# Kernel optimization log

Measured on AMD Instinct MI355X. Metric: run time of the kernel, lower is better.

## Reference

```python
import jax, jax.numpy as jnp
import numpy as np

N = 32768; D = 384; P = 3; CORR_D = 2 * 49 * P * P  # 882
G_KK = 4096; G_JK = 512
EPS = 1e-3  # LayerNorm eps in the torch module

FLOAT_NAMES = ("net","inp","corr","corr_w1","corr_b1","corr_w2","corr_b2","corr_ln_g","corr_ln_b","corr_w3","corr_b3","norm_g","norm_b","c1_w1","c1_b1","c1_w2","c1_b2","c2_w1","c2_b1","c2_w2","c2_b2","kk_fw","kk_fb","kk_gw","kk_gb","kk_hw","kk_hb","ij_fw","ij_fb","ij_gw","ij_gb","ij_hw","ij_hb","g_ln1_g","g_ln1_b","g1_gw","g1_gb","g1_r1w","g1_r1b","g1_r2w","g1_r2b","g_ln2_g","g_ln2_b","g2_gw","g2_gb","g2_r1w","g2_r1b","g2_r2w","g2_r2b","d_w","d_b","w_w","w_b")

def _ln(x, g, b):
    m = jnp.mean(x, -1, keepdims=True)
    v = jnp.mean((x - m) ** 2, -1, keepdims=True)
    return (x - m) * jax.lax.rsqrt(v + EPS) * g + b

def _mlp2(x, w1, b1, w2, b2):
    return jax.nn.relu(x @ w1 + b1) @ w2 + b2

def _gated_residual(x, gw, gb, r1w, r1b, r2w, r2b):
    gate = jax.nn.sigmoid(x @ gw + gb)
    res = jax.nn.relu(x @ r1w + r1b) @ r2w + r2b
    return x + gate * res

def _soft_agg(x, jx, fw, fb, gw, gb, hw, hb, num_groups):
    # x: [N, D]; jx: [N] group ids -> group-wise softmax weighted sum
    logits = x @ gw + gb
    feats = x @ fw + fb
    gmax = jax.ops.segment_max(logits, jx, num_segments=num_groups)
    e = jnp.exp(logits - gmax[jx])
    den = jax.ops.segment_sum(e, jx, num_segments=num_groups)
    w = e / (den[jx] + 1e-12)
    y = jax.ops.segment_sum(feats * w, jx, num_segments=num_groups)
    return (y @ hw + hb)[jx]

def _forward(p, nix, njx, ukk, ujk):
    # corr encoder MLP
    h = jax.nn.relu(p["corr"] @ p["corr_w1"] + p["corr_b1"]) @ p["corr_w2"] + p["corr_b2"]
    h = jax.nn.relu(_ln(h, p["corr_ln_g"], p["corr_ln_b"])) @ p["corr_w3"] + p["corr_b3"]
    net = p["net"] + p["inp"] + h
    net = _ln(net, p["norm_g"], p["norm_b"])
    mask_ix = (nix >= 0).astype(net.dtype).reshape(1, -1, 1)
    mask_jx = (njx >= 0).astype(net.dtype).reshape(1, -1, 1)
    net = net + _mlp2(mask_ix * net[:, nix], p["c1_w1"], p["c1_b1"], p["c1_w2"], p["c1_b2"])
    net = net + _mlp2(mask_jx * net[:, njx], p["c2_w1"], p["c2_b1"], p["c2_w2"], p["c2_b2"])
    net = net + _soft_agg(net[0], ukk, p["kk_fw"], p["kk_fb"], p["kk_gw"], p["kk_gb"], p["kk_hw"], p["kk_hb"], G_KK)[None]
    net = net + _soft_agg(net[0], ujk, p["ij_fw"], p["ij_fb"], p["ij_gw"], p["ij_gb"], p["ij_hw"], p["ij_hb"], G_JK)[None]
    net = _ln(net, p["g_ln1_g"], p["g_ln1_b"])
    net = _gated_residual(net, p["g1_gw"], p["g1_gb"], p["g1_r1w"], p["g1_r1b"], p["g1_r2w"], p["g1_r2b"])
    net = _ln(net, p["g_ln2_g"], p["g_ln2_b"])
    net = _gated_residual(net, p["g2_gw"], p["g2_gb"], p["g2_r1w"], p["g2_r1b"], p["g2_r2w"], p["g2_r2b"])
    r = jax.nn.relu(net)
    d = r @ p["d_w"] + p["d_b"]               # GradClip is identity in forward
    w = jax.nn.sigmoid(r @ p["w_w"] + p["w_b"])
    return net, d, w

def setup_inputs() -> dict:
    key = jax.random.key(0)
    it = iter(jax.random.split(key, 64))
    def pr(*shape):
        return jax.random.normal(next(it), shape, dtype=jnp.float32) * 0.02
    z = lambda *s: jnp.zeros(s, jnp.float32)
    o = lambda *s: jnp.ones(s, jnp.float32)
    inp = {
        "net": jax.random.normal(next(it), (1, N, D), dtype=jnp.float32),
        "inp": jax.random.normal(next(it), (1, N, D), dtype=jnp.float32),
        "corr": jax.random.normal(next(it), (1, N, CORR_D), dtype=jnp.float32),
        "nix": jax.random.randint(next(it), (N,), 0, N),
        "njx": jax.random.randint(next(it), (N,), 0, N),
        "ukk": jax.random.randint(next(it), (N,), 0, G_KK),
        "ujk": jax.random.randint(next(it), (N,), 0, G_JK),
        "corr_w1": pr(CORR_D, D), "corr_b1": z(D), "corr_w2": pr(D, D), "corr_b2": z(D),
        "corr_ln_g": o(D), "corr_ln_b": z(D), "corr_w3": pr(D, D), "corr_b3": z(D),
        "norm_g": o(D), "norm_b": z(D),
        "c1_w1": pr(D, D), "c1_b1": z(D), "c1_w2": pr(D, D), "c1_b2": z(D),
        "c2_w1": pr(D, D), "c2_b1": z(D), "c2_w2": pr(D, D), "c2_b2": z(D),
        "kk_fw": pr(D, D), "kk_fb": z(D), "kk_gw": pr(D, D), "kk_gb": z(D), "kk_hw": pr(D, D), "kk_hb": z(D),
        "ij_fw": pr(D, D), "ij_fb": z(D), "ij_gw": pr(D, D), "ij_gb": z(D), "ij_hw": pr(D, D), "ij_hb": z(D),
        "g_ln1_g": o(D), "g_ln1_b": z(D),
        "g1_gw": pr(D, D), "g1_gb": z(D), "g1_r1w": pr(D, D), "g1_r1b": z(D), "g1_r2w": pr(D, D), "g1_r2b": z(D),
        "g_ln2_g": o(D), "g_ln2_b": z(D),
        "g2_gw": pr(D, D), "g2_gb": z(D), "g2_r1w": pr(D, D), "g2_r1b": z(D), "g2_r2w": pr(D, D), "g2_r2b": z(D),
        "d_w": pr(D, 2), "d_b": z(2), "w_w": pr(D, 2), "w_b": z(2),
    }
    return inp

def reference(net, inp, corr, corr_w1, corr_b1, corr_w2, corr_b2, corr_ln_g, corr_ln_b, corr_w3, corr_b3, norm_g, norm_b, c1_w1, c1_b1, c1_w2, c1_b2, c2_w1, c2_b1, c2_w2, c2_b2, kk_fw, kk_fb, kk_gw, kk_gb, kk_hw, kk_hb, ij_fw, ij_fb, ij_gw, ij_gb, ij_hw, ij_hb, g_ln1_g, g_ln1_b, g1_gw, g1_gb, g1_r1w, g1_r1b, g1_r2w, g1_r2b, g_ln2_g, g_ln2_b, g2_gw, g2_gb, g2_r1w, g2_r1b, g2_r2w, g2_r2b, d_w, d_b, w_w, w_b, nix, njx, ukk, ujk):
    loc = locals()
    fl = {k: loc[k] for k in FLOAT_NAMES}
    return _forward(fl, nix, njx, ukk, ujk)
```

## Files before the change

kernel.cpp:

```cpp
#include <hip/hip_runtime.h>
#include <hip/hip_bf16.h>
#include <math.h>

#define NR 32768
#define DD 384
#define CDM 882
#define CDMP 896

typedef float f4 __attribute__((ext_vector_type(4)));
typedef float f32x4 __attribute__((ext_vector_type(4)));
typedef __bf16 bf16x8 __attribute__((ext_vector_type(8)));
typedef __bf16 bf16x4 __attribute__((ext_vector_type(4)));

__device__ inline f4 ld4(const float* p) { f4 v; __builtin_memcpy(&v, p, 16); return v; }
__device__ inline void st4(float* p, f4 v) { __builtin_memcpy(p, &v, 16); }
__device__ inline bf16x8 ld8h(const __bf16* p) { bf16x8 v; __builtin_memcpy(&v, p, 16); return v; }
__device__ inline void st8h(__bf16* p, bf16x8 v) { __builtin_memcpy(p, &v, 16); }

__device__ inline void gl_lds16(const void* g, void* l) {
  __builtin_amdgcn_global_load_lds(
      (const __attribute__((address_space(1))) void*)g,
      (__attribute__((address_space(3))) void*)l, 16, 0, 0);
}

__device__ inline float gred16(float v) {
#pragma unroll
  for (int o = 1; o < 16; o <<= 1) v += __shfl_xor(v, o, 64);
  return v;
}

__device__ inline int xcd_swz(int orig, int nwg) {
  int q = nwg >> 3, r = nwg & 7, xcd = orig & 7, lid = orig >> 3;
  return (xcd < r ? xcd * (q + 1) : r * (q + 1) + (xcd - r) * q) + lid;
}

__global__ __launch_bounds__(256) void corr2bf16_k(const float* __restrict__ src,
                                                   __bf16* __restrict__ dst) {
  int i = blockIdx.x * 256 + threadIdx.x;
  int row = i / 112, c8 = (i - row * 112) * 8;
  const float* sp = src + (size_t)row * CDM + c8;
  bf16x8 h;
  if (c8 + 8 <= CDM) {
#pragma unroll
    for (int e = 0; e < 8; ++e) h[e] = (__bf16)sp[e];
  } else {
#pragma unroll
    for (int e = 0; e < 8; ++e) h[e] = (c8 + e < CDM) ? (__bf16)sp[e] : (__bf16)0.f;
  }
  st8h(dst + (size_t)row * CDMP + c8, h);
}

struct WPtrs { const float* w[18]; };

__global__ __launch_bounds__(256) void trans_all_k(WPtrs P, __bf16* __restrict__ dst) {
  int wi = blockIdx.y;
  const float* W = P.w[wi];
  __bf16* WT = dst + (size_t)wi * DD * DD;
  int i = blockIdx.x * 256 + threadIdx.x;
  if (i >= DD * DD) return;
  int n = i / DD, k = i - n * DD;
  WT[i] = (__bf16)W[(size_t)k * DD + n];
}

__global__ __launch_bounds__(256) void trans_corr_k(const float* __restrict__ W,
                                                    __bf16* __restrict__ WT) {
  int i = blockIdx.x * 256 + threadIdx.x;
  if (i >= DD * CDMP) return;
  int n = i / CDMP, k = i - n * CDMP;
  WT[i] = (k < CDM) ? (__bf16)W[(size_t)k * DD + n] : (__bf16)0.f;
}

struct GP {
  const void* A; const __bf16* WT; const float* bias; __bf16* OUT;
  const __bf16* XRES; const __bf16* GIN;
  const float* p0; const float* p1; const float* p2; const float* p3;
  float* fout; const float* net32; const float* inp32;
  const int* idx; const __bf16* zpage; int M; int K;
};

template <int EPI>
__device__ __forceinline__ void epilogue(const GP& gp, f32x4 (&acc)[4][6],
                                         __bf16* sm, int m0, int w, int lane) {
  const int fr = lane & 15, fq = lane >> 4;
  const int wr = (w >> 2) * 64, wc = (w & 3) * 96;
  const int nw = w & 3;
  float bcol[6];
#pragma unroll
  for (int ni = 0; ni < 6; ++ni) bcol[ni] = gp.bias[wc + ni * 16 + fr];
#pragma unroll
  for (int mi = 0; mi < 4; ++mi)
#pragma unroll
    for (int ni = 0; ni < 6; ++ni)
#pragma unroll
      for (int j = 0; j < 4; ++j) acc[mi][ni][j] += bcol[ni];

  if constexpr (EPI <= 2) {
#pragma unroll
    for (int mi = 0; mi < 4; ++mi)
#pragma unroll
      for (int ni = 0; ni < 6; ++ni) {
        int col = wc + ni * 16 + fr;
#pragma unroll
        for (int j = 0; j < 4; ++j) {
          int row = m0 + wr + mi * 16 + fq * 4 + j;
          size_t o = (size_t)row * DD + col;
          float v = acc[mi][ni][j];
          if constexpr (EPI == 0) gp.OUT[o] = (__bf16)v;
          else if constexpr (EPI == 1) gp.OUT[o] = (__bf16)fmaxf(v, 0.f);
          else gp.OUT[o] = (__bf16)((float)gp.OUT[o] + v);
        }
      }
  } else {
    if constexpr (EPI == 5) {
#pragma unroll
      for (int mi = 0; mi < 4; ++mi)
#pragma unroll
        for (int ni = 0; ni < 6; ++ni) {
          int col = wc + ni * 16 + fr;
#pragma unroll
          for (int j = 0; j < 4; ++j) {
            int row = m0 + wr + mi * 16 + fq * 4 + j;
            size_t o = (size_t)row * DD + col;
            acc[mi][ni][j] += gp.net32[o] + gp.inp32[o];
          }
        }
    }
    if constexpr (EPI == 6 || EPI == 7) {
#pragma unroll
      for (int mi = 0; mi < 4; ++mi)
#pragma unroll
        for (int ni = 0; ni < 6; ++ni) {
          int col = wc + ni * 16 + fr;
#pragma unroll
          for (int j = 0; j < 4; ++j) {
            int row = m0 + wr + mi * 16 + fq * 4 + j;
            size_t o = (size_t)row * DD + col;
            float gl = (float)gp.GIN[o];
            float sg = 1.f / (1.f + expf(-gl));
            acc[mi][ni][j] = (float)gp.XRES[o] + sg * acc[mi][ni][j];
          }
        }
    }
    __syncthreads();
    if constexpr (EPI != 7) {
      float s1[4][4], s2[4][4];
#pragma unroll
      for (int mi = 0; mi < 4; ++mi)
#pragma unroll
        for (int j = 0; j < 4; ++j) { s1[mi][j] = 0.f; s2[mi][j] = 0.f; }
#pragma unroll
      for (int mi = 0; mi < 4; ++mi)
#pragma unroll
        for (int ni = 0; ni < 6; ++ni)
#pragma unroll
          for (int j = 0; j < 4; ++j) {
            float v = acc[mi][ni][j];
            s1[mi][j] += v;
            s2[mi][j] += v * v;
          }
#pragma unroll
      for (int o = 1; o < 16; o <<= 1)
#pragma unroll
        for (int mi = 0; mi < 4; ++mi)
#pragma unroll
          for (int j = 0; j < 4; ++j) {
            s1[mi][j] += __shfl_xor(s1[mi][j], o, 64);
            s2[mi][j] += __shfl_xor(s2[mi][j], o, 64);
          }
      float* lsum = (float*)sm;
      float* lsq = lsum + 512;
      if (fr == 0) {
#pragma unroll
        for (int mi = 0; mi < 4; ++mi)
#pragma unroll
          for (int j = 0; j < 4; ++j) {
            int rr = wr + mi * 16 + fq * 4 + j;
            lsum[rr * 4 + nw] = s1[mi][j];
            lsq[rr * 4 + nw] = s2[mi][j];
          }
      }
      __syncthreads();
      float mn[4][4], rs[4][4];
#pragma unroll
      for (int mi = 0; mi < 4; ++mi)
#pragma unroll
        for (int j = 0; j < 4; ++j) {
          int rr = wr + mi * 16 + fq * 4 + j;
          float S1 = lsum[rr * 4] + lsum[rr * 4 + 1] + lsum[rr * 4 + 2] + lsum[rr * 4 + 3];
          float S2 = lsq[rr * 4] + lsq[rr * 4 + 1] + lsq[rr * 4 + 2] + lsq[rr * 4 + 3];
          float m = S1 * (1.f / 384.f);
          float va = S2 * (1.f / 384.f) - m * m;
          mn[mi][j] = m;
          rs[mi][j] = rsqrtf(va + 1e-3f);
        }
#pragma unroll
      for (int ni = 0; ni < 6; ++ni) {
        int col = wc + ni * 16 + fr;
        float gg = gp.p0[col], bb = gp.p1[col];
#pragma unroll
        for (int mi = 0; mi < 4; ++mi)
#pragma unroll
          for (int j = 0; j < 4; ++j) {
            int row = m0 + wr + mi * 16 + fq * 4 + j;
            float y = (acc[mi][ni][j] - mn[mi][j]) * rs[mi][j] * gg + bb;
            if constexpr (EPI == 4) y = fmaxf(y, 0.f);
            gp.OUT[(size_t)row * DD + col] = (__bf16)y;
          }
      }
    } else {
      float c0[6], c1[6], c2[6], c3[6];
#pragma unroll
      for (int ni = 0; ni < 6; ++ni) {
        int col = wc + ni * 16 + fr;
        c0[ni] = gp.p0[2 * col];
        c1[ni] = gp.p0[2 * col + 1];
        c2[ni] = gp.p2[2 * col];
        c3[ni] = gp.p2[2 * col + 1];
      }
      float dt[4][4][4];
#pragma unroll
      for (int mi = 0; mi < 4; ++mi)
#pragma unroll
        for (int j = 0; j < 4; ++j)
#pragma unroll
          for (int q = 0; q < 4; ++q) dt[mi][j][q] = 0.f;
#pragma unroll
      for (int mi = 0; mi < 4; ++mi)
#pragma unroll
        for (int ni = 0; ni < 6; ++ni) {
          int col = wc + ni * 16 + fr;
#pragma unroll
          for (int j = 0; j < 4; ++j) {
            int row = m0 + wr + mi * 16 + fq * 4 + j;
            float v = acc[mi][ni][j];
            gp.fout[(size_t)row * DD + col] = v;
            float r = fmaxf(v, 0.f);
            dt[mi][j][0] += r * c0[ni];
            dt[mi][j][1] += r * c1[ni];
            dt[mi][j][2] += r * c2[ni];
            dt[mi][j][3] += r * c3[ni];
          }
        }
#pragma unroll
      for (int o = 1; o < 16; o <<= 1)
#pragma unroll
        for (int mi = 0; mi < 4; ++mi)
#pragma unroll
          for (int j = 0; j < 4; ++j)
#pragma unroll
            for (int q = 0; q < 4; ++q)
              dt[mi][j][q] += __shfl_xor(dt[mi][j][q], o, 64);
      float* lt = (float*)sm;
      if (fr == 0) {
#pragma unroll
        for (int mi = 0; mi < 4; ++mi)
#pragma unroll
          for (int j = 0; j < 4; ++j) {
            int rr = wr + mi * 16 + fq * 4 + j;
#pragma unroll
            for (int q = 0; q < 4; ++q) lt[(rr * 4 + nw) * 4 + q] = dt[mi][j][q];
          }
      }
      __syncthreads();
      if (nw == 0 && fr == 0) {
        float* fd = gp.fout + (size_t)NR * DD;
        float* fw = fd + (size_t)NR * 2;
#pragma unroll
        for (int mi = 0; mi < 4; ++mi)
#pragma unroll
          for (int j = 0; j < 4; ++j) {
            int rr = wr + mi * 16 + fq * 4 + j;
            int row = m0 + rr;
            float T[4];
#pragma unroll
            for (int q = 0; q < 4; ++q)
              T[q] = lt[(rr * 4 + 0) * 4 + q] + lt[(rr * 4 + 1) * 4 + q] +
                     lt[(rr * 4 + 2) * 4 + q] + lt[(rr * 4 + 3) * 4 + q];
            fd[2 * row] = T[0] + gp.p1[0];
            fd[2 * row + 1] = T[1] + gp.p1[1];
            fw[2 * row] = 1.f / (1.f + expf(-(T[2] + gp.p3[0])));
            fw[2 * row + 1] = 1.f / (1.f + expf(-(T[3] + gp.p3[1])));
          }
      }
    }
  }
}

__device__ __forceinline__ void mfma_block(const __bf16* As, const __bf16* Bs,
                                           f32x4 (&acc)[4][6], int wr, int wc,
                                           int fr, int fq) {
#pragma unroll
  for (int kk2 = 0; kk2 < 2; ++kk2) {
    bf16x8 af[4];
    bf16x8 bv[6];
#pragma unroll
    for (int mi = 0; mi < 4; ++mi) {
      int rr = wr + mi * 16 + fr;
      af[mi] = *reinterpret_cast<const bf16x8*>(
          &As[rr * 64 + (((fq + kk2 * 4) ^ (rr & 7)) << 3)]);
    }
#pragma unroll
    for (int ni = 0; ni < 6; ++ni) {
      int rr = wc + ni * 16 + fr;
      bv[ni] = *reinterpret_cast<const bf16x8*>(
          &Bs[rr * 64 + (((fq + kk2 * 4) ^ (rr & 7)) << 3)]);
    }
    __builtin_amdgcn_s_setprio(1);
#pragma unroll
    for (int mi = 0; mi < 4; ++mi)
#pragma unroll
      for (int ni = 0; ni < 6; ++ni)
        acc[mi][ni] = __builtin_amdgcn_mfma_f32_16x16x32_bf16(af[mi], bv[ni],
                                                              acc[mi][ni], 0, 0, 0);
    __builtin_amdgcn_s_setprio(0);
  }
}

template <int EPI, int AFP32>
__global__ __launch_bounds__(512, 1) void gemm_k(GP gp) {
  __shared__ __align__(16) __bf16 sm[2 * 32768];
  const int t = threadIdx.x;
  const int w = t >> 6, lane = t & 63;
  const int m0 = xcd_swz(blockIdx.x, gridDim.x) * 128;
  const int fr = lane & 15, fq = lane >> 4;
  const int wr = (w >> 2) * 64, wc = (w & 3) * 96;
  const int K = gp.K;

  const __bf16* aptr[2];
  int aadv[2];
  const __bf16* bptr[6];
#pragma unroll
  for (int j = 0; j < 2; ++j) {
    int rloc = w * 16 + j * 8 + (lane >> 3);
    int cch = (lane & 7) ^ (rloc & 7);
    if constexpr (!AFP32) {
      int ar = gp.idx ? gp.idx[m0 + rloc] : (m0 + rloc);
      if (ar >= 0) { aptr[j] = (const __bf16*)gp.A + (size_t)ar * K + cch * 8; aadv[j] = 64; }
      else { aptr[j] = gp.zpage; aadv[j] = 0; }
    }
  }
#pragma unroll
  for (int j = 0; j < 6; ++j) {
    int rloc = w * 48 + j * 8 + (lane >> 3);
    int cch = (lane & 7) ^ (rloc & 7);
    bptr[j] = gp.WT + (size_t)rloc * K + cch * 8;
  }
  const float* Af = (const float*)gp.A;
  const int NT = K >> 6;

  f32x4 acc[4][6];
#pragma unroll
  for (int a = 0; a < 4; ++a)
#pragma unroll
    for (int b = 0; b < 6; ++b)
#pragma unroll
      for (int j = 0; j < 4; ++j) acc[a][b][j] = 0.f;

  auto stageG = [&](int buf) {
    __bf16* As = sm + buf * 32768;
    __bf16* Bs = As + 8192;
#pragma unroll
    for (int j = 0; j < 2; ++j) {
      gl_lds16(aptr[j], &As[(w * 16 + j * 8) * 64]);
      aptr[j] += aadv[j];
    }
#pragma unroll
    for (int j = 0; j < 6; ++j) {
      gl_lds16(bptr[j], &Bs[(w * 48 + j * 8) * 64]);
      bptr[j] += 64;
    }
  };

  auto stageF = [&](int k0) {
    __bf16* As = sm;
    __bf16* Bs = sm + 8192;
#pragma unroll
    for (int j = 0; j < 2; ++j) {
      int rr = (t >> 3) + 64 * j;
      int cc = t & 7;
      const float* ap = Af + (size_t)(m0 + rr) * K + k0 + cc * 8;
      f4 v0 = ld4(ap), v1 = ld4(ap + 4);
      bf16x8 h;
#pragma unroll
      for (int e = 0; e < 4; ++e) { h[e] = (__bf16)v0[e]; h[4 + e] = (__bf16)v1[e]; }
      *reinterpret_cast<bf16x8*>(&As[rr * 64 + ((cc ^ (rr & 7)) << 3)]) = h;
    }
#pragma unroll
    for (int j = 0; j < 6; ++j) {
      gl_lds16(bptr[j], &Bs[(w * 48 + j * 8) * 64]);
      bptr[j] += 64;
    }
  };

  if constexpr (AFP32) {
    for (int tt = 0; tt < NT; ++tt) {
      if (tt) __syncthreads();
      stageF(tt << 6);
      __syncthreads();
      mfma_block(sm, sm + 8192, acc, wr, wc, fr, fq);
    }
  } else {
    stageG(0);
    int buf = 0;
    for (int tt = 0; tt < NT; ++tt) {
      if (tt + 1 < NT) {
        stageG(buf ^ 1);
        asm volatile("s_waitcnt vmcnt(8)" ::: "memory");
      } else {
        asm volatile("s_waitcnt vmcnt(0)" ::: "memory");
      }
      __builtin_amdgcn_s_barrier();
      __builtin_amdgcn_sched_barrier(0);
      mfma_block(sm + buf * 32768, sm + buf * 32768 + 8192, acc, wr, wc, fr, fq);
      __builtin_amdgcn_s_barrier();
      __builtin_amdgcn_sched_barrier(0);
      buf ^= 1;
    }
  }
  epilogue<EPI>(gp, acc, sm, m0, w, lane);
}

template <int EPIA, int EPIB>
__global__ __launch_bounds__(512, 2) void gemm2_k(GP ga, GP gb) {
  __shared__ __align__(16) __bf16 sm[32768];
  const int t = threadIdx.x;
  const int w = t >> 6, lane = t & 63;
  int wg = xcd_swz(blockIdx.x, gridDim.x);
  const int role = wg & 1;
  const int m0 = (wg >> 1) * 128;
  const GP& gp = role ? gb : ga;
  const int fr = lane & 15, fq = lane >> 4;
  const int wr = (w >> 2) * 64, wc = (w & 3) * 96;
  const int K = gp.K;

  const __bf16* aptr[2];
  const __bf16* bptr[6];
#pragma unroll
  for (int j = 0; j < 2; ++j) {
    int rloc = w * 16 + j * 8 + (lane >> 3);
    int cch = (lane & 7) ^ (rloc & 7);
    aptr[j] = (const __bf16*)gp.A + (size_t)(m0 + rloc) * K + cch * 8;
  }
#pragma unroll
  for (int j = 0; j < 6; ++j) {
    int rloc = w * 48 + j * 8 + (lane >> 3);
    int cch = (lane & 7) ^ (rloc & 7);
    bptr[j] = gp.WT + (size_t)rloc * K + cch * 8;
  }
  const int NT = K >> 6;

  f32x4 acc[4][6];
#pragma unroll
  for (int a = 0; a < 4; ++a)
#pragma unroll
    for (int b = 0; b < 6; ++b)
#pragma unroll
      for (int j = 0; j < 4; ++j) acc[a][b][j] = 0.f;

  for (int tt = 0; tt < NT; ++tt) {
    if (tt) __syncthreads();
#pragma unroll
    for (int j = 0; j < 2; ++j) {
      gl_lds16(aptr[j], &sm[(w * 16 + j * 8) * 64]);
      aptr[j] += 64;
    }
#pragma unroll
    for (int j = 0; j < 6; ++j) {
      gl_lds16(bptr[j], &sm[8192 + (w * 48 + j * 8) * 64]);
      bptr[j] += 64;
    }
    __syncthreads();
    mfma_block(sm, sm + 8192, acc, wr, wc, fr, fq);
  }
  if (role == 0) epilogue<EPIA>(gp, acc, sm, m0, w, lane);
  else epilogue<EPIB>(gp, acc, sm, m0, w, lane);
}

__global__ __launch_bounds__(256) void ln_ag_k(const __bf16* __restrict__ X,
                                               const __bf16* __restrict__ z,
                                               const int* __restrict__ gid,
                                               const float* __restrict__ g,
                                               const float* __restrict__ b,
                                               __bf16* __restrict__ out) {
  int w = threadIdx.x >> 6, lane = threadIdx.x & 63;
  int s = lane & 15, qq = lane >> 4;
  int row = blockIdx.x * 16 + w * 4 + qq;
  int gr = gid[row];
  size_t base = (size_t)row * DD;
  size_t zbase = (size_t)gr * DD;
  float v[24];
#pragma unroll
  for (int i = 0; i < 3; ++i) {
    int col = (s + 16 * i) * 8;
    bf16x8 h = ld8h(X + base + col);
    bf16x8 zz = ld8h(z + zbase + col);
#pragma unroll
    for (int e = 0; e < 8; ++e) v[i * 8 + e] = (float)h[e] + (float)zz[e];
  }
  float sm = 0.f;
#pragma unroll
  for (int i = 0; i < 24; ++i) sm += v[i];
  sm = gred16(sm);
  float mean = sm * (1.f / 384.f);
  float qs = 0.f;
#pragma unroll
  for (int i = 0; i < 24; ++i) { float d = v[i] - mean; qs += d * d; }
  qs = gred16(qs);
  float rs = rsqrtf(qs * (1.f / 384.f) + 1e-3f);
#pragma unroll
  for (int i = 0; i < 3; ++i) {
    int col = (s + 16 * i) * 8;
    f4 g0 = ld4(g + col), g1 = ld4(g + col + 4);
    f4 b0 = ld4(b + col), b1 = ld4(b + col + 4);
    bf16x8 o;
#pragma unroll
    for (int e = 0; e < 4; ++e) {
      o[e] = (__bf16)((v[i * 8 + e] - mean) * rs * g0[e] + b0[e]);
      o[4 + e] = (__bf16)((v[i * 8 + 4 + e] - mean) * rs * g1[e] + b1[e]);
    }
    st8h(out + base + col, o);
  }
}

__global__ __launch_bounds__(256) void hist2_k(const int* __restrict__ ukk,
                                               const int* __restrict__ ujk,
                                               int* __restrict__ ckk,
                                               int* __restrict__ cij) {
  int i = blockIdx.x * 256 + threadIdx.x;
  atomicAdd(&ckk[ukk[i]], 1);
  atomicAdd(&cij[ujk[i]], 1);
}

__device__ inline void scan_body(const int* cnt, int* off, int* curb, int G, int* ls) {
  int t = threadIdx.x;
  int per = G / 256;
  int base = t * per;
  int s = 0;
  for (int i = 0; i < per; ++i) s += cnt[base + i];
  ls[t] = s;
  __syncthreads();
  for (int o = 1; o < 256; o <<= 1) {
    int v = (t >= o) ? ls[t - o] : 0;
    __syncthreads();
    ls[t] += v;
    __syncthreads();
  }
  int run = (t == 0) ? 0 : ls[t - 1];
  for (int i = 0; i < per; ++i) {
    off[base + i] = run;
    run += cnt[base + i];
    curb[base + i] = 0;
  }
  if (t == 255) off[G] = run;
}

__global__ __launch_bounds__(256) void scan2_k(const int* ckk, int* okk, int* qkk,
                                               const int* cij, int* oij, int* qij) {
  __shared__ int ls[256];
  if (blockIdx.x == 0) scan_body(ckk, okk, qkk, 4096, ls);
  else scan_body(cij, oij, qij, 512, ls);
}

__global__ __launch_bounds__(256) void scatter2_k(const int* __restrict__ ukk,
                                                  const int* __restrict__ ujk,
                                                  const int* __restrict__ okk,
                                                  int* __restrict__ qkk,
                                                  int* __restrict__ rkk,
                                                  const int* __restrict__ oij,
                                                  int* __restrict__ qij,
                                                  int* __restrict__ rij) {
  int i = blockIdx.x * 256 + threadIdx.x;
  int g1 = ukk[i];
  rkk[okk[g1] + atomicAdd(&qkk[g1], 1)] = i;
  int g2 = ujk[i];
  rij[oij[g2] + atomicAdd(&qij[g2], 1)] = i;
}

__global__ __launch_bounds__(384) void segagg_k(const __bf16* __restrict__ L,
                                                const __bf16* __restrict__ Ft,
                                                const int* __restrict__ rows,
                                                const int* __restrict__ off,
                                                float* __restrict__ yb) {
  int g = blockIdx.x;
  int c = threadIdx.x;
  int s = off[g], e = off[g + 1];
  float mx = -3.0e38f;
  for (int p = s; p < e; ++p) {
    int r = rows[p];
    mx = fmaxf(mx, (float)L[(size_t)r * DD + c]);
  }
  float num = 0.f, den = 0.f;
  for (int p = s; p < e; ++p) {
    int r = rows[p];
    float lv = (float)L[(size_t)r * DD + c];
    float fv = (float)Ft[(size_t)r * DD + c];
    float ev = expf(lv - mx);
    den += ev;
    num += fv * ev;
  }
  yb[(size_t)g * DD + c] = num / (den + 1e-12f);
}

__global__ __launch_bounds__(256) void addgather_k(__bf16* __restrict__ X,
                                                   const __bf16* __restrict__ z,
                                                   const int* __restrict__ gid) {
  int i = blockIdx.x * 256 + threadIdx.x;
  int row = i / 48, c = (i - row * 48) * 8;
  int g = gid[row];
  size_t lo = (size_t)row * DD + c;
  bf16x8 a = ld8h(X + lo);
  bf16x8 zz = ld8h(z + (size_t)g * DD + c);
  bf16x8 o;
#pragma unroll
  for (int e = 0; e < 8; ++e) o[e] = (__bf16)((float)a[e] + (float)zz[e]);
  st8h(X + lo, o);
}

extern "C" void kernel_launch(void* const* d_in, const int* in_sizes, int n_in,
                              void* d_out, int out_size, void* d_ws, size_t ws_size,
                              hipStream_t stream) {
  const float* in_net = (const float*)d_in[0];
  const float* in_inp = (const float*)d_in[1];
  const float* in_corr = (const float*)d_in[2];
  const int* nix = (const int*)d_in[3];
  const int* njx = (const int*)d_in[4];
  const int* ukk = (const int*)d_in[5];
  const int* ujk = (const int*)d_in[6];
  auto F = [&](int i) { return (const float*)d_in[i]; };

  constexpr size_t MiB = 1024 * 1024;
  constexpr size_t SZ_ACT = (size_t)NR * DD * 2;
  char* ws = (char*)d_ws;
  __bf16* Xc = (__bf16*)(ws);
  __bf16* T2b = (__bf16*)(ws);
  __bf16* Fb = (__bf16*)(ws + SZ_ACT);
  __bf16* zb = (__bf16*)(ws + 2 * SZ_ACT);
  float* yb = (float*)(ws + 2 * SZ_ACT + 3 * MiB);
  __bf16* T1b = (__bf16*)(ws + 60 * MiB);
  char* p = ws + 84 * MiB;
  int* rows_kk = (int*)p; p += (size_t)NR * 4;
  int* rows_ij = (int*)p; p += (size_t)NR * 4;
  int* off_kk = (int*)p; p += 8192 * 4;
  int* off_ij = (int*)p; p += 1024 * 4;
  int* cnt_kk = (int*)p; p += 4096 * 4;
  int* cnt_ij = (int*)p; p += 512 * 4;
  int* curb_kk = (int*)p; p += 4096 * 4;
  int* curb_ij = (int*)p; p += 512 * 4;
  __bf16* wt_all = (__bf16*)p; p += (size_t)18 * DD * DD * 2;
  __bf16* wt_corr1 = (__bf16*)p; p += (size_t)DD * CDMP * 2;
  __bf16* zpage = (__bf16*)p;

  const int widx[18] = {17, 19, 21, 23, 25, 27, 29, 31, 33, 35, 39, 41, 43, 47, 49, 51, 9, 13};
  WPtrs P;
  for (int i = 0; i < 18; ++i) P.w[i] = F(widx[i]);
  auto WTp = [&](int i) { return wt_all + (size_t)i * DD * DD; };

  hipMemsetAsync(zpage, 0, 256, stream);
  hipMemsetAsync(cnt_kk, 0, 4096 * 4, stream);
  hipMemsetAsync(cnt_ij, 0, 512 * 4, stream);
  trans_all_k<<<dim3(576, 18), 256, 0, stream>>>(P, wt_all);
  trans_corr_k<<<1344, 256, 0, stream>>>(F(7), wt_corr1);
  corr2bf16_k<<<NR * 112 / 256, 256, 0, stream>>>(in_corr, Xc);
  hist2_k<<<NR / 256, 256, 0, stream>>>(ukk, ujk, cnt_kk, cnt_ij);
  scan2_k<<<2, 256, 0, stream>>>(cnt_kk, off_kk, curb_kk, cnt_ij, off_ij, curb_ij);
  scatter2_k<<<NR / 256, 256, 0, stream>>>(ukk, ujk, off_kk, curb_kk, rows_kk,
                                           off_ij, curb_ij, rows_ij);

  auto mkGP = [&](const void* A, const __bf16* WT, const float* bias, __bf16* OUT,
                  const __bf16* XRES, const __bf16* GIN, const float* p0,
                  const float* p1, const float* p2, const float* p3, float* fout,
                  const float* n32, const float* i32, const int* idx, int M, int K) {
    return GP{A, WT, bias, OUT, XRES, GIN, p0, p1, p2, p3, fout, n32, i32, idx, zpage, M, K};
  };

  auto G = [&](int epi, const void* A, const __bf16* WT, const float* bias,
               __bf16* OUT, const __bf16* XRES, const __bf16* GIN,
               const float* p0, const float* p1, const float* p2, const float* p3,
               float* fout, const float* n32, const float* i32,
               const int* idx, int M, int K) {
    GP gp = mkGP(A, WT, bias, OUT, XRES, GIN, p0, p1, p2, p3, fout, n32, i32, idx, M, K);
    dim3 g(M / 128), b(512);
    switch (epi) {
      case 1: gemm_k<1, 0><<<g, b, 0, stream>>>(gp); break;
      case 2: gemm_k<2, 0><<<g, b, 0, stream>>>(gp); break;
      case 4: gemm_k<4, 0><<<g, b, 0, stream>>>(gp); break;
      case 5: gemm_k<5, 0><<<g, b, 0, stream>>>(gp); break;
      case 6: gemm_k<6, 0><<<g, b, 0, stream>>>(gp); break;
      case 7: gemm_k<7, 0><<<g, b, 0, stream>>>(gp); break;
      case 8: gemm_k<0, 1><<<g, b, 0, stream>>>(gp); break;
    }
  };
  auto G2 = [&](const void* A, const __bf16* WTa, const float* ba, __bf16* Oa,
                const __bf16* WTb, const float* bb, __bf16* Ob, int epib, int M) {
    GP ga = mkGP(A, WTa, ba, Oa, nullptr, nullptr, nullptr, nullptr, nullptr,
                 nullptr, nullptr, nullptr, nullptr, nullptr, M, DD);
    GP gb = mkGP(A, WTb, bb, Ob, nullptr, nullptr, nullptr, nullptr, nullptr,
                 nullptr, nullptr, nullptr, nullptr, nullptr, M, DD);
    dim3 g(2 * (M / 128)), b(512);
    if (epib == 0) gemm2_k<0, 0><<<g, b, 0, stream>>>(ga, gb);
    else gemm2_k<0, 1><<<g, b, 0, stream>>>(ga, gb);
  };

  const int SEGB = NR * 48 / 256;

  G(1, Xc, wt_corr1, F(8), T1b, nullptr, nullptr, nullptr, nullptr, nullptr,
    nullptr, nullptr, nullptr, nullptr, nullptr, NR, CDMP);
  G(4, T1b, WTp(16), F(10), T2b, nullptr, nullptr, F(11), F(12), nullptr, nullptr,
    nullptr, nullptr, nullptr, nullptr, NR, DD);
  G(5, T2b, WTp(17), F(14), T1b, nullptr, nullptr, F(15), F(16), nullptr, nullptr,
    nullptr, in_net, in_inp, nullptr, NR, DD);
  G(1, T1b, WTp(0), F(18), T2b, nullptr, nullptr, nullptr, nullptr, nullptr,
    nullptr, nullptr, nullptr, nullptr, nix, NR, DD);
  G(2, T2b, WTp(1), F(20), T1b, nullptr, nullptr, nullptr, nullptr, nullptr,
    nullptr, nullptr, nullptr, nullptr, nullptr, NR, DD);
  G(1, T1b, WTp(2), F(22), T2b, nullptr, nullptr, nullptr, nullptr, nullptr,
    nullptr, nullptr, nullptr, nullptr, njx, NR, DD);
  G(2, T2b, WTp(3), F(24), T1b, nullptr, nullptr, nullptr, nullptr, nullptr,
    nullptr, nullptr, nullptr, nullptr, nullptr, NR, DD);
  G2(T1b, WTp(5), F(28), T2b, WTp(4), F(26), Fb, 0, NR);
  segagg_k<<<4096, 384, 0, stream>>>(T2b, Fb, rows_kk, off_kk, yb);
  G(8, yb, WTp(6), F(30), zb, nullptr, nullptr, nullptr, nullptr, nullptr,
    nullptr, nullptr, nullptr, nullptr, nullptr, 4096, DD);
  addgather_k<<<SEGB, 256, 0, stream>>>(T1b, zb, ukk);
  G2(T1b, WTp(8), F(34), T2b, WTp(7), F(32), Fb, 0, NR);
  segagg_k<<<512, 384, 0, stream>>>(T2b, Fb, rows_ij, off_ij, yb);
  G(8, yb, WTp(9), F(36), zb, nullptr, nullptr, nullptr, nullptr, nullptr,
    nullptr, nullptr, nullptr, nullptr, nullptr, 512, DD);
  ln_ag_k<<<NR / 16, 256, 0, stream>>>(T1b, zb, ujk, F(37), F(38), T2b);
  G2(T2b, WTp(10), F(40), Fb, WTp(11), F(42), T1b, 1, NR);
  G(6, T1b, WTp(12), F(44), T2b, T2b, Fb, F(45), F(46), nullptr, nullptr,
    nullptr, nullptr, nullptr, nullptr, NR, DD);
  G2(T2b, WTp(13), F(48), Fb, WTp(14), F(50), T1b, 1, NR);
  G(7, T1b, WTp(15), F(52), nullptr, T2b, Fb, F(53), F(54), F(55), F(56),
    (float*)d_out, nullptr, nullptr, nullptr, NR, DD);
}
```

Baseline: 634.6 us.

## Fuse back-to-back GEMM chains keeping intermediate activations in LDS

Adds chain2/chain3 kernels: the first GEMM writes its ReLU (or LN+ReLU) output as a 128x384 bf16 panel into shared memory, and the next GEMM reads A from that panel while streaming weights. This removes the global round-trips and launches between the MLP layers. The paired two-output gemm2 kernel is replaced by two separate gemm_k launches, and setprio around the MFMAs is dropped. In exchange it needs larger LDS (one block per CU) and uses a simpler weight-staging pipeline in the second phase.

```diff
diff --git a/kernel.cpp b/kernel.cpp
--- a/kernel.cpp
+++ b/kernel.cpp
@@ -107,7 +107,7 @@
           float v = acc[mi][ni][j];
           if constexpr (EPI == 0) gp.OUT[o] = (__bf16)v;
           else if constexpr (EPI == 1) gp.OUT[o] = (__bf16)fmaxf(v, 0.f);
-          else gp.OUT[o] = (__bf16)((float)gp.OUT[o] + v);
+          else gp.OUT[o] = (__bf16)((float)gp.XRES[o] + v);
         }
       }
   } else {
@@ -203,7 +203,6 @@
           for (int j = 0; j < 4; ++j) {
             int row = m0 + wr + mi * 16 + fq * 4 + j;
             float y = (acc[mi][ni][j] - mn[mi][j]) * rs[mi][j] * gg + bb;
-            if constexpr (EPI == 4) y = fmaxf(y, 0.f);
             gp.OUT[(size_t)row * DD + col] = (__bf16)y;
           }
       }
@@ -305,14 +304,223 @@
       bv[ni] = *reinterpret_cast<const bf16x8*>(
           &Bs[rr * 64 + (((fq + kk2 * 4) ^ (rr & 7)) << 3)]);
     }
-    __builtin_amdgcn_s_setprio(1);
 #pragma unroll
     for (int mi = 0; mi < 4; ++mi)
 #pragma unroll
       for (int ni = 0; ni < 6; ++ni)
         acc[mi][ni] = __builtin_amdgcn_mfma_f32_16x16x32_bf16(af[mi], bv[ni],
                                                               acc[mi][ni], 0, 0, 0);
-    __builtin_amdgcn_s_setprio(0);
+  }
+}
+
+__device__ __forceinline__ void zero_acc(f32x4 (&acc)[4][6]) {
+#pragma unroll
+  for (int a = 0; a < 4; ++a)
+#pragma unroll
+    for (int b = 0; b < 6; ++b)
+#pragma unroll
+      for (int j = 0; j < 4; ++j) acc[a][b][j] = 0.f;
+}
+
+__device__ __forceinline__ void phase1_run(const GP& gp, f32x4 (&acc)[4][6],
+                                           __bf16* sm, int m0, int t, int w,
+                                           int lane, int NT) {
+  const int fr = lane & 15, fq = lane >> 4;
+  const int wr = (w >> 2) * 64, wc = (w & 3) * 96;
+  const int K = gp.K;
+  const __bf16* aptr[2];
+  int aadv[2];
+  const __bf16* bptr[6];
+#pragma unroll
+  for (int j = 0; j < 2; ++j) {
+    int rloc = w * 16 + j * 8 + (lane >> 3);
+    int cch = (lane & 7) ^ (rloc & 7);
+    int ar = gp.idx ? gp.idx[m0 + rloc] : (m0 + rloc);
+    if (ar >= 0) { aptr[j] = (const __bf16*)gp.A + (size_t)ar * K + cch * 8; aadv[j] = 64; }
+    else { aptr[j] = gp.zpage; aadv[j] = 0; }
+  }
+#pragma unroll
+  for (int j = 0; j < 6; ++j) {
+    int rloc = w * 48 + j * 8 + (lane >> 3);
+    int cch = (lane & 7) ^ (rloc & 7);
+    bptr[j] = gp.WT + (size_t)rloc * K + cch * 8;
+  }
+  auto stageG = [&](int buf) {
+    __bf16* As = sm + buf * 32768;
+    __bf16* Bs = As + 8192;
+#pragma unroll
+    for (int j = 0; j < 2; ++j) {
+      gl_lds16(aptr[j], &As[(w * 16 + j * 8) * 64]);
+      aptr[j] += aadv[j];
+    }
+#pragma unroll
+    for (int j = 0; j < 6; ++j) {
+      gl_lds16(bptr[j], &Bs[(w * 48 + j * 8) * 64]);
+      bptr[j] += 64;
+    }
+  };
+  stageG(0);
+  int buf = 0;
+  for (int tt = 0; tt < NT; ++tt) {
+    if (tt + 1 < NT) {
+      stageG(buf ^ 1);
+      asm volatile("s_waitcnt vmcnt(8)" ::: "memory");
+    } else {
+      asm volatile("s_waitcnt vmcnt(0)" ::: "memory");
+    }
+    __builtin_amdgcn_s_barrier();
+    __builtin_amdgcn_sched_barrier(0);
+    mfma_block(sm + buf * 32768, sm + buf * 32768 + 8192, acc, wr, wc, fr, fq);
+    __builtin_amdgcn_s_barrier();
+    __builtin_amdgcn_sched_barrier(0);
+    buf ^= 1;
+  }
+}
+
+template <int MIDLN>
+__device__ __forceinline__ void epi_to_panel(const GP& gp, f32x4 (&acc)[4][6],
+                                             __bf16* sm, int w, int lane) {
+  const int fr = lane & 15, fq = lane >> 4;
+  const int wr = (w >> 2) * 64, wc = (w & 3) * 96;
+  const int nw = w & 3;
+  float bcol[6];
+#pragma unroll
+  for (int ni = 0; ni < 6; ++ni) bcol[ni] = gp.bias[wc + ni * 16 + fr];
+#pragma unroll
+  for (int mi = 0; mi < 4; ++mi)
+#pragma unroll
+    for (int ni = 0; ni < 6; ++ni)
+#pragma unroll
+      for (int j = 0; j < 4; ++j) acc[mi][ni][j] += bcol[ni];
+
+  float mn[4][4], rs[4][4];
+  if constexpr (MIDLN) {
+    float s1[4][4], s2[4][4];
+#pragma unroll
+    for (int mi = 0; mi < 4; ++mi)
+#pragma unroll
+      for (int j = 0; j < 4; ++j) { s1[mi][j] = 0.f; s2[mi][j] = 0.f; }
+#pragma unroll
+    for (int mi = 0; mi < 4; ++mi)
+#pragma unroll
+      for (int ni = 0; ni < 6; ++ni)
+#pragma unroll
+        for (int j = 0; j < 4; ++j) {
+          float v = acc[mi][ni][j];
+          s1[mi][j] += v;
+          s2[mi][j] += v * v;
+        }
+#pragma unroll
+    for (int o = 1; o < 16; o <<= 1)
+#pragma unroll
+      for (int mi = 0; mi < 4; ++mi)
+#pragma unroll
+        for (int j = 0; j < 4; ++j) {
+          s1[mi][j] += __shfl_xor(s1[mi][j], o, 64);
+          s2[mi][j] += __shfl_xor(s2[mi][j], o, 64);
+        }
+    float* lsum = (float*)(sm + 49152);
+    float* lsq = lsum + 512;
+    if (fr == 0) {
+#pragma unroll
+      for (int mi = 0; mi < 4; ++mi)
+#pragma unroll
+        for (int j = 0; j < 4; ++j) {
+          int rr = wr + mi * 16 + fq * 4 + j;
+          lsum[rr * 4 + nw] = s1[mi][j];
+          lsq[rr * 4 + nw] = s2[mi][j];
+        }
+    }
+    __syncthreads();
+#pragma unroll
+    for (int mi = 0; mi < 4; ++mi)
+#pragma unroll
+      for (int j = 0; j < 4; ++j) {
+        int rr = wr + mi * 16 + fq * 4 + j;
+        float S1 = lsum[rr * 4] + lsum[rr * 4 + 1] + lsum[rr * 4 + 2] + lsum[rr * 4 + 3];
+        float S2 = lsq[rr * 4] + lsq[rr * 4 + 1] + lsq[rr * 4 + 2] + lsq[rr * 4 + 3];
+        float m = S1 * (1.f / 384.f);
+        float va = S2 * (1.f / 384.f) - m * m;
+        mn[mi][j] = m;
+        rs[mi][j] = rsqrtf(va + 1e-3f);
+      }
+  }
+#pragma unroll
+  for (int ni = 0; ni < 6; ++ni) {
+    int cc = wc + ni * 16 + fr;
+    float gg = 1.f, bb = 0.f;
+    if constexpr (MIDLN) { gg = gp.p0[cc]; bb = gp.p1[cc]; }
+    int chunk = cc >> 3, ce = cc & 7;
+#pragma unroll
+    for (int mi = 0; mi < 4; ++mi)
+#pragma unroll
+      for (int j = 0; j < 4; ++j) {
+        int rr = wr + mi * 16 + fq * 4 + j;
+        float y = acc[mi][ni][j];
+        if constexpr (MIDLN) y = (y - mn[mi][j]) * rs[mi][j] * gg + bb;
+        y = fmaxf(y, 0.f);
+        sm[rr * 384 + ((chunk ^ (rr & 7)) << 3) + ce] = (__bf16)y;
+      }
+  }
+  __syncthreads();
+}
+
+__device__ __forceinline__ void phaseL_run(const GP& gp, f32x4 (&acc)[4][6],
+                                           __bf16* sm, int t, int w, int lane) {
+  const int fr = lane & 15, fq = lane >> 4;
+  const int wr = (w >> 2) * 64, wc = (w & 3) * 96;
+  __bf16* Bs = sm + 49152;
+  int rloc[6];
+  const __bf16* bptr[6];
+#pragma unroll
+  for (int j = 0; j < 6; ++j) {
+    rloc[j] = w * 48 + j * 8 + (lane >> 3);
+    int cch = (lane & 7) ^ (rloc[j] & 7);
+    bptr[j] = gp.WT + (size_t)rloc[j] * DD + cch * 8;
+  }
+#pragma unroll
+  for (int j = 0; j < 6; ++j) {
+    gl_lds16(bptr[j], &Bs[(w * 48 + j * 8) * 64]);
+    bptr[j] += 64;
+  }
+  asm volatile("s_waitcnt vmcnt(0)" ::: "memory");
+  __builtin_amdgcn_s_barrier();
+  __builtin_amdgcn_sched_barrier(0);
+  for (int tt = 0; tt < 6; ++tt) {
+    bf16x8 r[6];
+    if (tt < 5) {
+#pragma unroll
+      for (int j = 0; j < 6; ++j) { r[j] = ld8h(bptr[j]); bptr[j] += 64; }
+    }
+#pragma unroll
+    for (int kk2 = 0; kk2 < 2; ++kk2) {
+      bf16x8 af[4];
+      bf16x8 bv[6];
+#pragma unroll
+      for (int mi = 0; mi < 4; ++mi) {
+        int rr = wr + mi * 16 + fr;
+        af[mi] = *reinterpret_cast<const bf16x8*>(
+            &sm[rr * 384 + ((tt * 8 + ((kk2 * 4 + fq) ^ (rr & 7))) << 3)]);
+      }
+#pragma unroll
+      for (int ni = 0; ni < 6; ++ni) {
+        int rr = wc + ni * 16 + fr;
+        bv[ni] = *reinterpret_cast<const bf16x8*>(
+            &Bs[rr * 64 + (((fq + kk2 * 4) ^ (rr & 7)) << 3)]);
+      }
+#pragma unroll
+      for (int mi = 0; mi < 4; ++mi)
+#pragma unroll
+        for (int ni = 0; ni < 6; ++ni)
+          acc[mi][ni] = __builtin_amdgcn_mfma_f32_16x16x32_bf16(af[mi], bv[ni],
+                                                                acc[mi][ni], 0, 0, 0);
+    }
+    __syncthreads();
+    if (tt < 5) {
+#pragma unroll
+      for (int j = 0; j < 6; ++j) st8h(&Bs[rloc[j] * 64 + (lane & 7) * 8], r[j]);
+      __syncthreads();
+    }
   }
 }
 
@@ -324,156 +532,78 @@
   const int m0 = xcd_swz(blockIdx.x, gridDim.x) * 128;
   const int fr = lane & 15, fq = lane >> 4;
   const int wr = (w >> 2) * 64, wc = (w & 3) * 96;
-  const int K = gp.K;
-
-  const __bf16* aptr[2];
-  int aadv[2];
-  const __bf16* bptr[6];
-#pragma unroll
-  for (int j = 0; j < 2; ++j) {
-    int rloc = w * 16 + j * 8 + (lane >> 3);
-    int cch = (lane & 7) ^ (rloc & 7);
-    if constexpr (!AFP32) {
-      int ar = gp.idx ? gp.idx[m0 + rloc] : (m0 + rloc);
-      if (ar >= 0) { aptr[j] = (const __bf16*)gp.A + (size_t)ar * K + cch * 8; aadv[j] = 64; }
-      else { aptr[j] = gp.zpage; aadv[j] = 0; }
-    }
-  }
-#pragma unroll
-  for (int j = 0; j < 6; ++j) {
-    int rloc = w * 48 + j * 8 + (lane >> 3);
-    int cch = (lane & 7) ^ (rloc & 7);
-    bptr[j] = gp.WT + (size_t)rloc * K + cch * 8;
-  }
-  const float* Af = (const float*)gp.A;
-  const int NT = K >> 6;
-
   f32x4 acc[4][6];
-#pragma unroll
-  for (int a = 0; a < 4; ++a)
-#pragma unroll
-    for (int b = 0; b < 6; ++b)
-#pragma unroll
-      for (int j = 0; j < 4; ++j) acc[a][b][j] = 0.f;
-
-  auto stageG = [&](int buf) {
-    __bf16* As = sm + buf * 32768;
-    __bf16* Bs = As + 8192;
-#pragma unroll
-    for (int j = 0; j < 2; ++j) {
-      gl_lds16(aptr[j], &As[(w * 16 + j * 8) * 64]);
-      aptr[j] += aadv[j];
-    }
+  zero_acc(acc);
+  if constexpr (AFP32) {
+    const float* Af = (const float*)gp.A;
+    const int K = gp.K;
+    const __bf16* bptr[6];
 #pragma unroll
     for (int j = 0; j < 6; ++j) {
-      gl_lds16(bptr[j], &Bs[(w * 48 + j * 8) * 64]);
-      bptr[j] += 64;
-    }
-  };
-
-  auto stageF = [&](int k0) {
-    __bf16* As = sm;
-    __bf16* Bs = sm + 8192;
-#pragma unroll
-    for (int j = 0; j < 2; ++j) {
-      int rr = (t >> 3) + 64 * j;
-      int cc = t & 7;
-      const float* ap = Af + (size_t)(m0 + rr) * K + k0 + cc * 8;
-      f4 v0 = ld4(ap), v1 = ld4(ap + 4);
-      bf16x8 h;
-#pragma unroll
-      for (int e = 0; e < 4; ++e) { h[e] = (__bf16)v0[e]; h[4 + e] = (__bf16)v1[e]; }
-      *reinterpret_cast<bf16x8*>(&As[rr * 64 + ((cc ^ (rr & 7)) << 3)]) = h;
-    }
-#pragma unroll
-    for (int j = 0; j < 6; ++j) {
-      gl_lds16(bptr[j], &Bs[(w * 48 + j * 8) * 64]);
-      bptr[j] += 64;
-    }
-  };
-
-  if constexpr (AFP32) {
+      int rloc = w * 48 + j * 8 + (lane >> 3);
+      int cch = (lane & 7) ^ (rloc & 7);
+      bptr[j] = gp.WT + (size_t)rloc * K + cch * 8;
+    }
+    const int NT = K >> 6;
     for (int tt = 0; tt < NT; ++tt) {
       if (tt) __syncthreads();
-      stageF(tt << 6);
+      __bf16* As = sm;
+      __bf16* Bs = sm + 8192;
+#pragma unroll
+      for (int j = 0; j < 2; ++j) {
+        int rr = (t >> 3) + 64 * j;
+        int cc = t & 7;
+        const float* ap = Af + (size_t)(m0 + rr) * K + (tt << 6) + cc * 8;
+        f4 v0 = ld4(ap), v1 = ld4(ap + 4);
+        bf16x8 h;
+#pragma unroll
+        for (int e = 0; e < 4; ++e) { h[e] = (__bf16)v0[e]; h[4 + e] = (__bf16)v1[e]; }
+        *reinterpret_cast<bf16x8*>(&As[rr * 64 + ((cc ^ (rr & 7)) << 3)]) = h;
+      }
+#pragma unroll
+      for (int j = 0; j < 6; ++j) {
+        gl_lds16(bptr[j], &Bs[(w * 48 + j * 8) * 64]);
+        bptr[j] += 64;
+      }
       __syncthreads();
       mfma_block(sm, sm + 8192, acc, wr, wc, fr, fq);
     }
   } else {
-    stageG(0);
-    int buf = 0;
-    for (int tt = 0; tt < NT; ++tt) {
-      if (tt + 1 < NT) {
-        stageG(buf ^ 1);
-        asm volatile("s_waitcnt vmcnt(8)" ::: "memory");
-      } else {
-        asm volatile("s_waitcnt vmcnt(0)" ::: "memory");
-      }
-      __builtin_amdgcn_s_barrier();
-      __builtin_amdgcn_sched_barrier(0);
-      mfma_block(sm + buf * 32768, sm + buf * 32768 + 8192, acc, wr, wc, fr, fq);
-      __builtin_amdgcn_s_barrier();
-      __builtin_amdgcn_sched_barrier(0);
-      buf ^= 1;
-    }
+    phase1_run(gp, acc, sm, m0, t, w, lane, gp.K >> 6);
   }
   epilogue<EPI>(gp, acc, sm, m0, w, lane);
 }
 
-template <int EPIA, int EPIB>
-__global__ __launch_bounds__(512, 2) void gemm2_k(GP ga, GP gb) {
-  __shared__ __align__(16) __bf16 sm[32768];
+template <int EPIL>
+__global__ __launch_bounds__(512, 1) void chain2_k(GP p1, GP p2) {
+  __shared__ __align__(16) __bf16 sm[73728];
   const int t = threadIdx.x;
   const int w = t >> 6, lane = t & 63;
-  int wg = xcd_swz(blockIdx.x, gridDim.x);
-  const int role = wg & 1;
-  const int m0 = (wg >> 1) * 128;
-  const GP& gp = role ? gb : ga;
-  const int fr = lane & 15, fq = lane >> 4;
-  const int wr = (w >> 2) * 64, wc = (w & 3) * 96;
-  const int K = gp.K;
-
-  const __bf16* aptr[2];
-  const __bf16* bptr[6];
-#pragma unroll
-  for (int j = 0; j < 2; ++j) {
-    int rloc = w * 16 + j * 8 + (lane >> 3);
-    int cch = (lane & 7) ^ (rloc & 7);
-    aptr[j] = (const __bf16*)gp.A + (size_t)(m0 + rloc) * K + cch * 8;
-  }
-#pragma unroll
-  for (int j = 0; j < 6; ++j) {
-    int rloc = w * 48 + j * 8 + (lane >> 3);
-    int cch = (lane & 7) ^ (rloc & 7);
-    bptr[j] = gp.WT + (size_t)rloc * K + cch * 8;
-  }
-  const int NT = K >> 6;
-
+  const int m0 = xcd_swz(blockIdx.x, gridDim.x) * 128;
   f32x4 acc[4][6];
-#pragma unroll
-  for (int a = 0; a < 4; ++a)
-#pragma unroll
-    for (int b = 0; b < 6; ++b)
-#pragma unroll
-      for (int j = 0; j < 4; ++j) acc[a][b][j] = 0.f;
-
-  for (int tt = 0; tt < NT; ++tt) {
-    if (tt) __syncthreads();
-#pragma unroll
-    for (int j = 0; j < 2; ++j) {
-      gl_lds16(aptr[j], &sm[(w * 16 + j * 8) * 64]);
-      aptr[j] += 64;
-    }
-#pragma unroll
-    for (int j = 0; j < 6; ++j) {
-      gl_lds16(bptr[j], &sm[8192 + (w * 48 + j * 8) * 64]);
-      bptr[j] += 64;
-    }
-    __syncthreads();
-    mfma_block(sm, sm + 8192, acc, wr, wc, fr, fq);
-  }
-  if (role == 0) epilogue<EPIA>(gp, acc, sm, m0, w, lane);
-  else epilogue<EPIB>(gp, acc, sm, m0, w, lane);
+  zero_acc(acc);
+  phase1_run(p1, acc, sm, m0, t, w, lane, p1.K >> 6);
+  epi_to_panel<0>(p1, acc, sm, w, lane);
+  zero_acc(acc);
+  phaseL_run(p2, acc, sm, t, w, lane);
+  epilogue<EPIL>(p2, acc, sm, m0, w, lane);
+}
+
+__global__ __launch_bounds__(512, 1) void chain3_k(GP p1, GP p2, GP p3) {
+  __shared__ __align__(16) __bf16 sm[73728];
+  const int t = threadIdx.x;
+  const int w = t >> 6, lane = t & 63;
+  const int m0 = xcd_swz(blockIdx.x, gridDim.x) * 128;
+  f32x4 acc[4][6];
+  zero_acc(acc);
+  phase1_run(p1, acc, sm, m0, t, w, lane, p1.K >> 6);
+  epi_to_panel<0>(p1, acc, sm, w, lane);
+  zero_acc(acc);
+  phaseL_run(p2, acc, sm, t, w, lane);
+  epi_to_panel<1>(p2, acc, sm, w, lane);
+  zero_acc(acc);
+  phaseL_run(p3, acc, sm, t, w, lane);
+  epilogue<5>(p3, acc, sm, m0, w, lane);
 }
 
 __global__ __launch_bounds__(256) void ln_ag_k(const __bf16* __restrict__ X,
@@ -672,65 +802,69 @@
                   const float* n32, const float* i32, const int* idx, int M, int K) {
     return GP{A, WT, bias, OUT, XRES, GIN, p0, p1, p2, p3, fout, n32, i32, idx, zpage, M, K};
   };
-
-  auto G = [&](int epi, const void* A, const __bf16* WT, const float* bias,
-               __bf16* OUT, const __bf16* XRES, const __bf16* GIN,
-               const float* p0, const float* p1, const float* p2, const float* p3,
-               float* fout, const float* n32, const float* i32,
-               const int* idx, int M, int K) {
-    GP gp = mkGP(A, WT, bias, OUT, XRES, GIN, p0, p1, p2, p3, fout, n32, i32, idx, M, K);
-    dim3 g(M / 128), b(512);
-    switch (epi) {
-      case 1: gemm_k<1, 0><<<g, b, 0, stream>>>(gp); break;
-      case 2: gemm_k<2, 0><<<g, b, 0, stream>>>(gp); break;
-      case 4: gemm_k<4, 0><<<g, b, 0, stream>>>(gp); break;
-      case 5: gemm_k<5, 0><<<g, b, 0, stream>>>(gp); break;
-      case 6: gemm_k<6, 0><<<g, b, 0, stream>>>(gp); break;
-      case 7: gemm_k<7, 0><<<g, b, 0, stream>>>(gp); break;
-      case 8: gemm_k<0, 1><<<g, b, 0, stream>>>(gp); break;
-    }
-  };
-  auto G2 = [&](const void* A, const __bf16* WTa, const float* ba, __bf16* Oa,
-                const __bf16* WTb, const float* bb, __bf16* Ob, int epib, int M) {
-    GP ga = mkGP(A, WTa, ba, Oa, nullptr, nullptr, nullptr, nullptr, nullptr,
-                 nullptr, nullptr, nullptr, nullptr, nullptr, M, DD);
-    GP gb = mkGP(A, WTb, bb, Ob, nullptr, nullptr, nullptr, nullptr, nullptr,
-                 nullptr, nullptr, nullptr, nullptr, nullptr, M, DD);
-    dim3 g(2 * (M / 128)), b(512);
-    if (epib == 0) gemm2_k<0, 0><<<g, b, 0, stream>>>(ga, gb);
-    else gemm2_k<0, 1><<<g, b, 0, stream>>>(ga, gb);
-  };
+  GP gnull = mkGP(nullptr, nullptr, nullptr, nullptr, nullptr, nullptr, nullptr,
+                  nullptr, nullptr, nullptr, nullptr, nullptr, nullptr, nullptr, 0, DD);
 
   const int SEGB = NR * 48 / 256;
-
-  G(1, Xc, wt_corr1, F(8), T1b, nullptr, nullptr, nullptr, nullptr, nullptr,
-    nullptr, nullptr, nullptr, nullptr, nullptr, NR, CDMP);
-  G(4, T1b, WTp(16), F(10), T2b, nullptr, nullptr, F(11), F(12), nullptr, nullptr,
-    nullptr, nullptr, nullptr, nullptr, NR, DD);
-  G(5, T2b, WTp(17), F(14), T1b, nullptr, nullptr, F(15), F(16), nullptr, nullptr,
-    nullptr, in_net, in_inp, nullptr, NR, DD);
-  G(1, T1b, WTp(0), F(18), T2b, nullptr, nullptr, nullptr, nullptr, nullptr,
-    nullptr, nullptr, nullptr, nullptr, nix, NR, DD);
-  G(2, T2b, WTp(1), F(20), T1b, nullptr, nullptr, nullptr, nullptr, nullptr,
-    nullptr, nullptr, nullptr, nullptr, nullptr, NR, DD);
-  G(1, T1b, WTp(2), F(22), T2b, nullptr, nullptr, nullptr, nullptr, nullptr,
-    nullptr, nullptr, nullptr, nullptr, njx, NR, DD);
-  G(2, T2b, WTp(3), F(24), T1b, nullptr, nullptr, nullptr, nullptr, nullptr,
-    nullptr, nullptr, nullptr, nullptr, nullptr, NR, DD);
-  G2(T1b, WTp(5), F(28), T2b, WTp(4), F(26), Fb, 0, NR);
+  const dim3 B512(512);
+  const dim3 GRNR(NR / 128);
+
+  {
+    GP p1 = gnull; p1.A = Xc; p1.WT = wt_corr1; p1.bias = F(8); p1.K = CDMP;
+    GP p2 = gnull; p2.WT = WTp(16); p2.bias = F(10); p2.p0 = F(11); p2.p1 = F(12);
+    GP p3 = gnull; p3.WT = WTp(17); p3.bias = F(14); p3.OUT = T1b;
+    p3.p0 = F(15); p3.p1 = F(16); p3.net32 = in_net; p3.inp32 = in_inp;
+    chain3_k<<<GRNR, B512, 0, stream>>>(p1, p2, p3);
+  }
+  {
+    GP p1 = gnull; p1.A = T1b; p1.WT = WTp(0); p1.bias = F(18); p1.idx = nix; p1.K = DD;
+    GP p2 = gnull; p2.WT = WTp(1); p2.bias = F(20); p2.XRES = T1b; p2.OUT = Fb;
+    chain2_k<2><<<GRNR, B512, 0, stream>>>(p1, p2);
+  }
+  {
+    GP p1 = gnull; p1.A = Fb; p1.WT = WTp(2); p1.bias = F(22); p1.idx = njx; p1.K = DD;
+    GP p2 = gnull; p2.WT = WTp(3); p2.bias = F(24); p2.XRES = Fb; p2.OUT = T1b;
+    chain2_k<2><<<GRNR, B512, 0, stream>>>(p1, p2);
+  }
+  {
+    GP g = gnull; g.A = T1b; g.WT = WTp(5); g.bias = F(28); g.OUT = T2b; g.K = DD;
+    gemm_k<0, 0><<<GRNR, B512, 0, stream>>>(g);
+    g.WT = WTp(4); g.bias = F(26); g.OUT = Fb;
+    gemm_k<0, 0><<<GRNR, B512, 0, stream>>>(g);
+  }
   segagg_k<<<4096, 384, 0, stream>>>(T2b, Fb, rows_kk, off_kk, yb);
-  G(8, yb, WTp(6), F(30), zb, nullptr, nullptr, nullptr, nullptr, nullptr,
-    nullptr, nullptr, nullptr, nullptr, nullptr, 4096, DD);
+  {
+    GP g = gnull; g.A = yb; g.WT = WTp(6); g.bias = F(30); g.OUT = zb; g.M = 4096; g.K = DD;
+    gemm_k<0, 1><<<dim3(32), B512, 0, stream>>>(g);
+  }
   addgather_k<<<SEGB, 256, 0, stream>>>(T1b, zb, ukk);
-  G2(T1b, WTp(8), F(34), T2b, WTp(7), F(32), Fb, 0, NR);
+  {
+    GP g = gnull; g.A = T1b; g.WT = WTp(8); g.bias = F(34); g.OUT = T2b; g.K = DD;
+    gemm_k<0, 0><<<GRNR, B512, 0, stream>>>(g);
+    g.WT = WTp(7); g.bias = F(32); g.OUT = Fb;
+    gemm_k<0, 0><<<GRNR, B512, 0, stream>>>(g);
+  }
   segagg_k<<<512, 384, 0, stream>>>(T2b, Fb, rows_ij, off_ij, yb);
-  G(8, yb, WTp(9), F(36), zb, nullptr, nullptr, nullptr, nullptr, nullptr,
-    nullptr, nullptr, nullptr, nullptr, nullptr, 512, DD);
+  {
+    GP g = gnull; g.A = yb; g.WT = WTp(9); g.bias = F(36); g.OUT = zb; g.M = 512; g.K = DD;
+    gemm_k<0, 1><<<dim3(4), B512, 0, stream>>>(g);
+  }
   ln_ag_k<<<NR / 16, 256, 0, stream>>>(T1b, zb, ujk, F(37), F(38), T2b);
-  G2(T2b, WTp(10), F(40), Fb, WTp(11), F(42), T1b, 1, NR);
-  G(6, T1b, WTp(12), F(44), T2b, T2b, Fb, F(45), F(46), nullptr, nullptr,
-    nullptr, nullptr, nullptr, nullptr, NR, DD);
-  G2(T2b, WTp(13), F(48), Fb, WTp(14), F(50), T1b, 1, NR);
-  G(7, T1b, WTp(15), F(52), nullptr, T2b, Fb, F(53), F(54), F(55), F(56),
-    (float*)d_out, nullptr, nullptr, nullptr, NR, DD);
-}
+  {
+    GP g = gnull; g.A = T2b; g.WT = WTp(10); g.bias = F(40); g.OUT = Fb; g.K = DD;
+    gemm_k<0, 0><<<GRNR, B512, 0, stream>>>(g);
+    GP p1 = gnull; p1.A = T2b; p1.WT = WTp(11); p1.bias = F(42); p1.K = DD;
+    GP p2 = gnull; p2.WT = WTp(12); p2.bias = F(44); p2.XRES = T2b; p2.GIN = Fb;
+    p2.p0 = F(45); p2.p1 = F(46); p2.OUT = T2b;
+    chain2_k<6><<<GRNR, B512, 0, stream>>>(p1, p2);
+  }
+  {
+    GP g = gnull; g.A = T2b; g.WT = WTp(13); g.bias = F(48); g.OUT = Fb; g.K = DD;
+    gemm_k<0, 0><<<GRNR, B512, 0, stream>>>(g);
+    GP p1 = gnull; p1.A = T2b; p1.WT = WTp(14); p1.bias = F(50); p1.K = DD;
+    GP p2 = gnull; p2.WT = WTp(15); p2.bias = F(52); p2.XRES = T2b; p2.GIN = Fb;
+    p2.p0 = F(53); p2.p1 = F(54); p2.p2 = F(55); p2.p3 = F(56);
+    p2.fout = (float*)d_out;
+    chain2_k<7><<<GRNR, B512, 0, stream>>>(p1, p2);
+  }
+}
```

Result: no change. 638.5 us (+0.6%).
